# Kernel optimization log

Measured on AMD Instinct MI355X. Metric: run time of the kernel, lower is better.

Reference implementation:

```python
import jax, jax.numpy as jnp
import numpy as np

N = 8192
LATENT_DIM = 64


def setup_inputs() -> dict:
    key = jax.random.key(0)
    kx, ky = jax.random.split(key)
    x = jax.random.normal(kx, (N, LATENT_DIM), dtype=jnp.float32)
    y = jax.random.normal(ky, (N, LATENT_DIM), dtype=jnp.float32)
    return {"x": x, "y": y}


def _rbf_kernel(a, b):
    # Faithful to torch: exp(-mean((a_i - b_j)^2, axis=dim) / dim)
    #                  = exp(-||a_i - b_j||^2 / dim^2)
    # Computed via the expanded-sq-dist identity to avoid the [N, N, dim]
    # tiled intermediate the torch code materializes.
    dim = a.shape[1]
    sq_a = jnp.sum(a * a, axis=1)  # [Na]
    sq_b = jnp.sum(b * b, axis=1)  # [Nb]
    sq_dist = sq_a[:, None] + sq_b[None, :] - 2.0 * (a @ b.T)  # [Na, Nb]
    return jnp.exp(-sq_dist / (dim * dim))


def reference(x, y):
    # MMD with RBF kernel: mean k(x,x) + mean k(y,y) - 2 mean k(x,y)
    kxx = jnp.mean(_rbf_kernel(x, x))
    kyy = jnp.mean(_rbf_kernel(y, y))
    kxy = jnp.mean(_rbf_kernel(x, y))
    return kxx + kyy - 2.0 * kxy
```

## Files before the change

### kernel.cpp

```cpp
#include <hip/hip_runtime.h>
#include <cmath>

#define NPTS 8192
#define DIM 64
#define BT 128

#define LEAF_F   0
#define LEAF_N   (3 * 8192 * 64)
#define ROWS_F   (LEAF_F + LEAF_N)
#define ROWS_N   (3 * 8192)
#define MEANS_F  (ROWS_F + ROWS_N)
#define NX_F     ((MEANS_F + 3 + 3) & ~3)
#define NY_F     (NX_F + 8192)
#define SPLIT_F  (NY_F + 8192)
#define SPLIT_ELEMS (NPTS * DIM)


typedef short bf16x8 __attribute__((ext_vector_type(8)));
typedef float f32x4  __attribute__((ext_vector_type(4)));

__device__ __forceinline__ unsigned short f32_bf16_rne(float f) {
    unsigned u = __float_as_uint(f);
    return (unsigned short)((u + 0x7FFFu + ((u >> 16) & 1u)) >> 16);
}
__device__ __forceinline__ float bf16_f32(unsigned short h) {
    return __uint_as_float(((unsigned)h) << 16);
}

__global__ void prep_kernel(const float* __restrict__ x, const float* __restrict__ y,
                            unsigned short* __restrict__ Xh, unsigned short* __restrict__ Xl,
                            unsigned short* __restrict__ Yh, unsigned short* __restrict__ Yl,
                            float* __restrict__ nx, float* __restrict__ ny) {
    int r = blockIdx.x * 64 + threadIdx.x;
    int isY = r >= NPTS;
    int rr = isY ? r - NPTS : r;
    const float4* Rg = (const float4*)((isY ? y : x) + (size_t)rr * DIM);
    unsigned short* Hh = isY ? Yh : Xh;
    unsigned short* Hl = isY ? Yl : Xl;
    const int t16 = rr >> 4, mrow = rr & 15;
    float s = 0.f;
    #pragma unroll
    for (int k4 = 0; k4 < 16; ++k4) {
        float4 v = Rg[k4];
        ushort4 h, l;
        h.x = f32_bf16_rne(v.x); l.x = f32_bf16_rne(v.x - bf16_f32(h.x));
        h.y = f32_bf16_rne(v.y); l.y = f32_bf16_rne(v.y - bf16_f32(h.y));
        h.z = f32_bf16_rne(v.z); l.z = f32_bf16_rne(v.z - bf16_f32(h.z));
        h.w = f32_bf16_rne(v.w); l.w = f32_bf16_rne(v.w - bf16_f32(h.w));
        int off = t16 * 1024 + (k4 >> 3) * 512 + ((k4 >> 1) & 3) * 128 + mrow * 8 + (k4 & 1) * 4;
        *(ushort4*)(Hh + off) = h;
        *(ushort4*)(Hl + off) = l;
        s = fmaf(v.x, v.x, s); s = fmaf(v.y, v.y, s);
        s = fmaf(v.z, v.z, s); s = fmaf(v.w, v.w, s);
    }
    if (isY) ny[rr] = s; else nx[rr] = s;
}

__global__ __launch_bounds__(512, 4) void mmd_tile_kernel(
    const unsigned short* __restrict__ Xh, const unsigned short* __restrict__ Xl,
    const unsigned short* __restrict__ Yh, const unsigned short* __restrict__ Yl,
    const float* __restrict__ nx, const float* __restrict__ ny,
    float* __restrict__ leafs)
{
    const int gi = blockIdx.x;
    const int gj = blockIdx.y;
    int zz, bx, by;
    if (blockIdx.z == 1) {
        if (gi >= 64) return;
        zz = 2; bx = gi; by = gj;
    } else if (gi > gj) {
        zz = 0; by = gj; bx = gi - 1;
    } else {
        zz = 1; by = gi; bx = gj;
    }

    __shared__ float sqA[BT];
    __shared__ float sqB[BT];
    __shared__ float rowpart[2][BT];
    __shared__ float colpart[4][BT];

    const int t = threadIdx.x;
    const size_t arow = (size_t)by * BT;
    const size_t brow = (size_t)bx * BT;
    const int cb = bx;

    const unsigned short* pAh = (zz == 1) ? Yh : Xh;
    const unsigned short* pAl = (zz == 1) ? Yl : Xl;
    const unsigned short* pBh = (zz == 0) ? Xh : Yh;
    const unsigned short* pBl = (zz == 0) ? Xl : Yl;

    if (t < 256) {
        const float* nA = (zz == 1) ? ny : nx;
        const float* nB = (zz == 0) ? nx : ny;
        if (t < BT) sqA[t] = nA[arow + t];
        else        sqB[t - BT] = nB[brow + t - BT];
    }
    __syncthreads();

    const int lane = t & 63;
    const int wv   = t >> 6;
    const int mrow = lane & 15;
    const int quad = lane >> 4;
    const int rblk = (wv & 3) << 5;
    const int cblk = (wv >> 2) << 6;

    const int aT = by * 8 + (wv & 3) * 2;
    const int bT = bx * 8 + (wv >> 2) * 4;
    const int lsub = quad * 128 + mrow * 8;

    bf16x8 fAh[2][2], fAl[2][2];
    #pragma unroll
    for (int rt = 0; rt < 2; ++rt)
        #pragma unroll
        for (int kc = 0; kc < 2; ++kc) {
            int off = (aT + rt) * 1024 + kc * 512 + lsub;
            fAh[rt][kc] = *(const bf16x8*)(pAh + off);
            fAl[rt][kc] = *(const bf16x8*)(pAl + off);
        }

    f32x4 acc[2][4];
    #pragma unroll
    for (int rt = 0; rt < 2; ++rt)
        #pragma unroll
        for (int ct = 0; ct < 4; ++ct)
            acc[rt][ct] = (f32x4){0.f, 0.f, 0.f, 0.f};

    #pragma unroll
    for (int ct = 0; ct < 4; ++ct) {
        int boff = (bT + ct) * 1024 + lsub;
        bf16x8 bh0 = *(const bf16x8*)(pBh + boff);
        bf16x8 bh1 = *(const bf16x8*)(pBh + boff + 512);
        bf16x8 bl0 = *(const bf16x8*)(pBl + boff);
        bf16x8 bl1 = *(const bf16x8*)(pBl + boff + 512);
        #pragma unroll
        for (int rt = 0; rt < 2; ++rt) {
            f32x4 c = acc[rt][ct];
            c = __builtin_amdgcn_mfma_f32_16x16x32_bf16(fAh[rt][0], bh0, c, 0, 0, 0);
            c = __builtin_amdgcn_mfma_f32_16x16x32_bf16(fAh[rt][0], bl0, c, 0, 0, 0);
            c = __builtin_amdgcn_mfma_f32_16x16x32_bf16(fAl[rt][0], bh0, c, 0, 0, 0);
            c = __builtin_amdgcn_mfma_f32_16x16x32_bf16(fAh[rt][1], bh1, c, 0, 0, 0);
            c = __builtin_amdgcn_mfma_f32_16x16x32_bf16(fAh[rt][1], bl1, c, 0, 0, 0);
            c = __builtin_amdgcn_mfma_f32_16x16x32_bf16(fAl[rt][1], bh1, c, 0, 0, 0);
            acc[rt][ct] = c;
        }
    }

    const float SCL = (float)(-1.4426950408889634 / 4096.0);
    float kk[2][4][4];
    #pragma unroll
    for (int rt = 0; rt < 2; ++rt)
        #pragma unroll
        for (int ct = 0; ct < 4; ++ct)
            #pragma unroll
            for (int i = 0; i < 4; ++i) {
                int row = rblk + rt * 16 + quad * 4 + i;
                int col = cblk + ct * 16 + mrow;
                float d  = acc[rt][ct][i];
                float s2 = sqA[row] + sqB[col];
                float sqd = s2 - 2.0f * d;
                kk[rt][ct][i] = exp2f(sqd * SCL);
            }

    const bool domirror = (zz < 2) && (bx > by);

    float rs[2][4];
    #pragma unroll
    for (int rt = 0; rt < 2; ++rt)
        #pragma unroll
        for (int i = 0; i < 4; ++i)
            rs[rt][i] = (kk[rt][0][i] + kk[rt][1][i]) + (kk[rt][2][i] + kk[rt][3][i]);

    float cs[4];
    if (domirror) {
        #pragma unroll
        for (int ct = 0; ct < 4; ++ct)
            cs[ct] = ((kk[0][ct][0] + kk[0][ct][1]) + (kk[0][ct][2] + kk[0][ct][3]))
                   + ((kk[1][ct][0] + kk[1][ct][1]) + (kk[1][ct][2] + kk[1][ct][3]));
    }

    const int b0 = lane & 1;
    const int b1 = (lane >> 1) & 1;
    const int b2 = (lane >> 2) & 1;
    const int b3 = (lane >> 3) & 1;

    float a4[4];
    #pragma unroll
    for (int i = 0; i < 4; ++i) {
        float snd = b3 ? rs[0][i] : rs[1][i];
        float rcv = __shfl_xor(snd, 8);
        a4[i] = (b3 ? rs[1][i] : rs[0][i]) + rcv;
    }
    float a2[2];
    #pragma unroll
    for (int j = 0; j < 2; ++j) {
        float snd = b2 ? a4[j] : a4[2 + j];
        float rcv = __shfl_xor(snd, 4);
        a2[j] = (b2 ? a4[2 + j] : a4[j]) + rcv;
    }
    {
        float snd = b1 ? a2[0] : a2[1];
        float rcv = __shfl_xor(snd, 2);
        float a1  = (b1 ? a2[1] : a2[0]) + rcv;
        float r64 = a1 + __shfl_xor(a1, 1);
        if (b0 == 0)
            rowpart[wv >> 2][rblk + b3 * 16 + quad * 4 + b2 * 2 + b1] = r64;
    }

    if (domirror) {
        const int b4 = (lane >> 4) & 1;
        const int b5 = (lane >> 5) & 1;
        float c2[2];
        #pragma unroll
        for (int j = 0; j < 2; ++j) {
            float snd = b4 ? cs[j] : cs[2 + j];
            float rcv = __shfl_xor(snd, 16);
            c2[j] = (b4 ? cs[2 + j] : cs[j]) + rcv;
        }
        float snd = b5 ? c2[0] : c2[1];
        float rcv = __shfl_xor(snd, 32);
        float c1  = (b5 ? c2[1] : c2[0]) + rcv;
        colpart[wv & 3][cblk + (b4 * 2 + b5) * 16 + mrow] = c1;
    }
    __syncthreads();

    if (t < BT) {
        leafs[((size_t)zz * 64 + cb) * 8192 + arow + t] = rowpart[0][t] + rowpart[1][t];
        if (domirror) {
            leafs[((size_t)zz * 64 + by) * 8192 + brow + t] =
                (colpart[0][t] + colpart[1][t]) + (colpart[2][t] + colpart[3][t]);
        }
    }
}

__global__ void rowsum_kernel(const float* __restrict__ leafs, float* __restrict__ rowsums) {
    const int t = threadIdx.x;
    const int tid = blockIdx.x * 256 + t;
    const int z = tid >> 13;
    const int r = tid & 8191;
    const float* base = leafs + ((size_t)z * 64) * 8192 + r;
    float v[64];
    #pragma unroll
    for (int cbi = 0; cbi < 64; ++cbi) v[cbi] = base[(size_t)cbi * 8192];
    #pragma unroll
    for (int n = 32; n >= 1; n >>= 1)
        #pragma unroll
        for (int i = 0; i < 64; ++i)
            if (i < n) v[i] = v[2*i] + v[2*i+1];
    rowsums[tid] = v[0];
}

__global__ void colsum_kernel(const float* __restrict__ rowsums, float* __restrict__ means) {
    __shared__ float L[256];
    const int z = blockIdx.x;
    const int t = threadIdx.x;
    const float4* src = (const float4*)(rowsums + z * 8192);
    float w[32];
    #pragma unroll
    for (int i = 0; i < 8; ++i) {
        float4 q = src[t * 8 + i];
        w[4*i+0] = q.x; w[4*i+1] = q.y; w[4*i+2] = q.z; w[4*i+3] = q.w;
    }
    #pragma unroll
    for (int n = 16; n >= 1; n >>= 1)
        #pragma unroll
        for (int i = 0; i < 32; ++i)
            if (i < n) w[i] = w[2*i] + w[2*i+1];
    L[t] = w[0];
    __syncthreads();
    for (int n = 128; n >= 1; n >>= 1) {
        float u = 0.f;
        if (t < n) u = L[2*t] + L[2*t+1];
        __syncthreads();
        if (t < n) L[t] = u;
        __syncthreads();
    }
    if (t == 0) means[z] = L[0] * (1.0f / 67108864.0f);
}

__global__ void combine_kernel(const float* __restrict__ means, float* __restrict__ out) {
    float t1 = means[0] + means[1];
    out[0] = t1 - 2.0f * means[2];
}

extern "C" void kernel_launch(void* const* d_in, const int* in_sizes, int n_in,
                              void* d_out, int out_size, void* d_ws, size_t ws_size,
                              hipStream_t stream) {
    const float* x = (const float*)d_in[0];
    const float* y = (const float*)d_in[1];
    float* wsf     = (float*)d_ws;
    float* leafs   = wsf + LEAF_F;
    float* rowsums = wsf + ROWS_F;
    float* means   = wsf + MEANS_F;
    float* nx      = wsf + NX_F;
    float* ny      = wsf + NY_F;
    unsigned short* Xh = (unsigned short*)(wsf + SPLIT_F);
    unsigned short* Xl = Xh + SPLIT_ELEMS;
    unsigned short* Yh = Xl + SPLIT_ELEMS;
    unsigned short* Yl = Yh + SPLIT_ELEMS;

    prep_kernel<<<256, 64, 0, stream>>>(x, y, Xh, Xl, Yh, Yl, nx, ny);
    dim3 grid(65, 64, 2);
    mmd_tile_kernel<<<grid, 512, 0, stream>>>(Xh, Xl, Yh, Yl, nx, ny, leafs);
    rowsum_kernel<<<96, 256, 0, stream>>>(leafs, rowsums);
    colsum_kernel<<<3, 256, 0, stream>>>(rowsums, means);
    combine_kernel<<<1, 1, 0, stream>>>(means, (float*)d_out);
}
```

Before: 146.5 us.

## Interleave MFMA with exp epilogue, hardware exp2, swizzle shuffles, fuse final reductions

The tile kernel now computes exp and row/column partial sums per column tile right after its MFMAs, so the full accumulator array no longer has to stay live. Squared norms are loaded directly into registers instead of through shared memory, which removes a barrier. exp2f is replaced with the raw v_exp_f32 instruction, and most xor shuffles are replaced with ds_swizzle. The colsum and combine kernels are merged into a single one-block launch, removing one kernel launch at the cost of serializing the three reductions.

```diff
diff --git a/kernel.cpp b/kernel.cpp
--- a/kernel.cpp
+++ b/kernel.cpp
@@ -26,6 +26,22 @@
 __device__ __forceinline__ float bf16_f32(unsigned short h) {
     return __uint_as_float(((unsigned)h) << 16);
 }
+
+__device__ __forceinline__ float exp2_hw(float x) {
+#if __has_builtin(__builtin_amdgcn_exp2f)
+    return __builtin_amdgcn_exp2f(x);
+#else
+    float r;
+    asm("v_exp_f32 %0, %1" : "=v"(r) : "v"(x));
+    return r;
+#endif
+}
+
+#define SWZ_XOR1(x)  __int_as_float(__builtin_amdgcn_ds_swizzle(__float_as_int(x), 0x041F))
+#define SWZ_XOR2(x)  __int_as_float(__builtin_amdgcn_ds_swizzle(__float_as_int(x), 0x081F))
+#define SWZ_XOR4(x)  __int_as_float(__builtin_amdgcn_ds_swizzle(__float_as_int(x), 0x101F))
+#define SWZ_XOR8(x)  __int_as_float(__builtin_amdgcn_ds_swizzle(__float_as_int(x), 0x201F))
+#define SWZ_XOR16(x) __int_as_float(__builtin_amdgcn_ds_swizzle(__float_as_int(x), 0x401F))
 
 __global__ void prep_kernel(const float* __restrict__ x, const float* __restrict__ y,
                             unsigned short* __restrict__ Xh, unsigned short* __restrict__ Xl,
@@ -74,8 +90,6 @@
         zz = 1; by = gi; bx = gj;
     }
 
-    __shared__ float sqA[BT];
-    __shared__ float sqB[BT];
     __shared__ float rowpart[2][BT];
     __shared__ float colpart[4][BT];
 
@@ -88,14 +102,8 @@
     const unsigned short* pAl = (zz == 1) ? Yl : Xl;
     const unsigned short* pBh = (zz == 0) ? Xh : Yh;
     const unsigned short* pBl = (zz == 0) ? Xl : Yl;
-
-    if (t < 256) {
-        const float* nA = (zz == 1) ? ny : nx;
-        const float* nB = (zz == 0) ? nx : ny;
-        if (t < BT) sqA[t] = nA[arow + t];
-        else        sqB[t - BT] = nB[brow + t - BT];
-    }
-    __syncthreads();
+    const float* nA = (zz == 1) ? ny : nx;
+    const float* nB = (zz == 0) ? nx : ny;
 
     const int lane = t & 63;
     const int wv   = t >> 6;
@@ -108,6 +116,19 @@
     const int bT = bx * 8 + (wv >> 2) * 4;
     const int lsub = quad * 128 + mrow * 8;
 
+    const bool domirror = (zz < 2) && (bx > by);
+
+    float sa[8];
+    #pragma unroll
+    for (int rt = 0; rt < 2; ++rt)
+        #pragma unroll
+        for (int i = 0; i < 4; ++i)
+            sa[rt * 4 + i] = nA[arow + rblk + rt * 16 + quad * 4 + i];
+    float sb[4];
+    #pragma unroll
+    for (int ct = 0; ct < 4; ++ct)
+        sb[ct] = nB[brow + cblk + ct * 16 + mrow];
+
     bf16x8 fAh[2][2], fAl[2][2];
     #pragma unroll
     for (int rt = 0; rt < 2; ++rt)
@@ -118,12 +139,10 @@
             fAl[rt][kc] = *(const bf16x8*)(pAl + off);
         }
 
-    f32x4 acc[2][4];
-    #pragma unroll
-    for (int rt = 0; rt < 2; ++rt)
-        #pragma unroll
-        for (int ct = 0; ct < 4; ++ct)
-            acc[rt][ct] = (f32x4){0.f, 0.f, 0.f, 0.f};
+    const float SCL = (float)(-1.4426950408889634 / 4096.0);
+    float rs01[2][4] = {{0.f,0.f,0.f,0.f},{0.f,0.f,0.f,0.f}};
+    float rs23[2][4] = {{0.f,0.f,0.f,0.f},{0.f,0.f,0.f,0.f}};
+    float cs[4];
 
     #pragma unroll
     for (int ct = 0; ct < 4; ++ct) {
@@ -132,51 +151,50 @@
         bf16x8 bh1 = *(const bf16x8*)(pBh + boff + 512);
         bf16x8 bl0 = *(const bf16x8*)(pBl + boff);
         bf16x8 bl1 = *(const bf16x8*)(pBl + boff + 512);
-        #pragma unroll
-        for (int rt = 0; rt < 2; ++rt) {
-            f32x4 c = acc[rt][ct];
-            c = __builtin_amdgcn_mfma_f32_16x16x32_bf16(fAh[rt][0], bh0, c, 0, 0, 0);
-            c = __builtin_amdgcn_mfma_f32_16x16x32_bf16(fAh[rt][0], bl0, c, 0, 0, 0);
-            c = __builtin_amdgcn_mfma_f32_16x16x32_bf16(fAl[rt][0], bh0, c, 0, 0, 0);
-            c = __builtin_amdgcn_mfma_f32_16x16x32_bf16(fAh[rt][1], bh1, c, 0, 0, 0);
-            c = __builtin_amdgcn_mfma_f32_16x16x32_bf16(fAh[rt][1], bl1, c, 0, 0, 0);
-            c = __builtin_amdgcn_mfma_f32_16x16x32_bf16(fAl[rt][1], bh1, c, 0, 0, 0);
-            acc[rt][ct] = c;
-        }
-    }
-
-    const float SCL = (float)(-1.4426950408889634 / 4096.0);
-    float kk[2][4][4];
+
+        f32x4 c0 = (f32x4){0.f, 0.f, 0.f, 0.f};
+        f32x4 c1 = (f32x4){0.f, 0.f, 0.f, 0.f};
+        c0 = __builtin_amdgcn_mfma_f32_16x16x32_bf16(fAh[0][0], bh0, c0, 0, 0, 0);
+        c0 = __builtin_amdgcn_mfma_f32_16x16x32_bf16(fAh[0][0], bl0, c0, 0, 0, 0);
+        c0 = __builtin_amdgcn_mfma_f32_16x16x32_bf16(fAl[0][0], bh0, c0, 0, 0, 0);
+        c0 = __builtin_amdgcn_mfma_f32_16x16x32_bf16(fAh[0][1], bh1, c0, 0, 0, 0);
+        c0 = __builtin_amdgcn_mfma_f32_16x16x32_bf16(fAh[0][1], bl1, c0, 0, 0, 0);
+        c0 = __builtin_amdgcn_mfma_f32_16x16x32_bf16(fAl[0][1], bh1, c0, 0, 0, 0);
+        c1 = __builtin_amdgcn_mfma_f32_16x16x32_bf16(fAh[1][0], bh0, c1, 0, 0, 0);
+        c1 = __builtin_amdgcn_mfma_f32_16x16x32_bf16(fAh[1][0], bl0, c1, 0, 0, 0);
+        c1 = __builtin_amdgcn_mfma_f32_16x16x32_bf16(fAl[1][0], bh0, c1, 0, 0, 0);
+        c1 = __builtin_amdgcn_mfma_f32_16x16x32_bf16(fAh[1][1], bh1, c1, 0, 0, 0);
+        c1 = __builtin_amdgcn_mfma_f32_16x16x32_bf16(fAh[1][1], bl1, c1, 0, 0, 0);
+        c1 = __builtin_amdgcn_mfma_f32_16x16x32_bf16(fAl[1][1], bh1, c1, 0, 0, 0);
+
+        float k0[4], k1[4];
+        #pragma unroll
+        for (int i = 0; i < 4; ++i) {
+            float d0  = c0[i];
+            float s20 = sa[i] + sb[ct];
+            k0[i] = exp2_hw((s20 - 2.0f * d0) * SCL);
+            float d1  = c1[i];
+            float s21 = sa[4 + i] + sb[ct];
+            k1[i] = exp2_hw((s21 - 2.0f * d1) * SCL);
+        }
+        if (ct < 2) {
+            #pragma unroll
+            for (int i = 0; i < 4; ++i) { rs01[0][i] += k0[i]; rs01[1][i] += k1[i]; }
+        } else {
+            #pragma unroll
+            for (int i = 0; i < 4; ++i) { rs23[0][i] += k0[i]; rs23[1][i] += k1[i]; }
+        }
+        if (domirror)
+            cs[ct] = ((k0[0] + k0[1]) + (k0[2] + k0[3]))
+                   + ((k1[0] + k1[1]) + (k1[2] + k1[3]));
+    }
+
+    float rs[2][4];
     #pragma unroll
     for (int rt = 0; rt < 2; ++rt)
         #pragma unroll
-        for (int ct = 0; ct < 4; ++ct)
-            #pragma unroll
-            for (int i = 0; i < 4; ++i) {
-                int row = rblk + rt * 16 + quad * 4 + i;
-                int col = cblk + ct * 16 + mrow;
-                float d  = acc[rt][ct][i];
-                float s2 = sqA[row] + sqB[col];
-                float sqd = s2 - 2.0f * d;
-                kk[rt][ct][i] = exp2f(sqd * SCL);
-            }
-
-    const bool domirror = (zz < 2) && (bx > by);
-
-    float rs[2][4];
-    #pragma unroll
-    for (int rt = 0; rt < 2; ++rt)
-        #pragma unroll
         for (int i = 0; i < 4; ++i)
-            rs[rt][i] = (kk[rt][0][i] + kk[rt][1][i]) + (kk[rt][2][i] + kk[rt][3][i]);
-
-    float cs[4];
-    if (domirror) {
-        #pragma unroll
-        for (int ct = 0; ct < 4; ++ct)
-            cs[ct] = ((kk[0][ct][0] + kk[0][ct][1]) + (kk[0][ct][2] + kk[0][ct][3]))
-                   + ((kk[1][ct][0] + kk[1][ct][1]) + (kk[1][ct][2] + kk[1][ct][3]));
-    }
+            rs[rt][i] = rs01[rt][i] + rs23[rt][i];
 
     const int b0 = lane & 1;
     const int b1 = (lane >> 1) & 1;
@@ -187,21 +205,21 @@
     #pragma unroll
     for (int i = 0; i < 4; ++i) {
         float snd = b3 ? rs[0][i] : rs[1][i];
-        float rcv = __shfl_xor(snd, 8);
+        float rcv = SWZ_XOR8(snd);
         a4[i] = (b3 ? rs[1][i] : rs[0][i]) + rcv;
     }
     float a2[2];
     #pragma unroll
     for (int j = 0; j < 2; ++j) {
         float snd = b2 ? a4[j] : a4[2 + j];
-        float rcv = __shfl_xor(snd, 4);
+        float rcv = SWZ_XOR4(snd);
         a2[j] = (b2 ? a4[2 + j] : a4[j]) + rcv;
     }
     {
         float snd = b1 ? a2[0] : a2[1];
-        float rcv = __shfl_xor(snd, 2);
+        float rcv = SWZ_XOR2(snd);
         float a1  = (b1 ? a2[1] : a2[0]) + rcv;
-        float r64 = a1 + __shfl_xor(a1, 1);
+        float r64 = a1 + SWZ_XOR1(a1);
         if (b0 == 0)
             rowpart[wv >> 2][rblk + b3 * 16 + quad * 4 + b2 * 2 + b1] = r64;
     }
@@ -213,13 +231,13 @@
         #pragma unroll
         for (int j = 0; j < 2; ++j) {
             float snd = b4 ? cs[j] : cs[2 + j];
-            float rcv = __shfl_xor(snd, 16);
+            float rcv = SWZ_XOR16(snd);
             c2[j] = (b4 ? cs[2 + j] : cs[j]) + rcv;
         }
         float snd = b5 ? c2[0] : c2[1];
         float rcv = __shfl_xor(snd, 32);
-        float c1  = (b5 ? c2[1] : c2[0]) + rcv;
-        colpart[wv & 3][cblk + (b4 * 2 + b5) * 16 + mrow] = c1;
+        float c1v = (b5 ? c2[1] : c2[0]) + rcv;
+        colpart[wv & 3][cblk + (b4 * 2 + b5) * 16 + mrow] = c1v;
     }
     __syncthreads();
 
@@ -249,37 +267,39 @@
     rowsums[tid] = v[0];
 }
 
-__global__ void colsum_kernel(const float* __restrict__ rowsums, float* __restrict__ means) {
+__global__ void colsum_kernel(const float* __restrict__ rowsums, float* __restrict__ out) {
     __shared__ float L[256];
-    const int z = blockIdx.x;
+    __shared__ float m[3];
     const int t = threadIdx.x;
-    const float4* src = (const float4*)(rowsums + z * 8192);
-    float w[32];
-    #pragma unroll
-    for (int i = 0; i < 8; ++i) {
-        float4 q = src[t * 8 + i];
-        w[4*i+0] = q.x; w[4*i+1] = q.y; w[4*i+2] = q.z; w[4*i+3] = q.w;
-    }
-    #pragma unroll
-    for (int n = 16; n >= 1; n >>= 1)
-        #pragma unroll
-        for (int i = 0; i < 32; ++i)
-            if (i < n) w[i] = w[2*i] + w[2*i+1];
-    L[t] = w[0];
-    __syncthreads();
-    for (int n = 128; n >= 1; n >>= 1) {
-        float u = 0.f;
-        if (t < n) u = L[2*t] + L[2*t+1];
+    for (int z = 0; z < 3; ++z) {
+        const float4* src = (const float4*)(rowsums + z * 8192);
+        float w[32];
+        #pragma unroll
+        for (int i = 0; i < 8; ++i) {
+            float4 q = src[t * 8 + i];
+            w[4*i+0] = q.x; w[4*i+1] = q.y; w[4*i+2] = q.z; w[4*i+3] = q.w;
+        }
+        #pragma unroll
+        for (int n = 16; n >= 1; n >>= 1)
+            #pragma unroll
+            for (int i = 0; i < 32; ++i)
+                if (i < n) w[i] = w[2*i] + w[2*i+1];
+        L[t] = w[0];
         __syncthreads();
-        if (t < n) L[t] = u;
+        for (int n = 128; n >= 1; n >>= 1) {
+            float u = 0.f;
+            if (t < n) u = L[2*t] + L[2*t+1];
+            __syncthreads();
+            if (t < n) L[t] = u;
+            __syncthreads();
+        }
+        if (t == 0) m[z] = L[0] * (1.0f / 67108864.0f);
         __syncthreads();
     }
-    if (t == 0) means[z] = L[0] * (1.0f / 67108864.0f);
-}
-
-__global__ void combine_kernel(const float* __restrict__ means, float* __restrict__ out) {
-    float t1 = means[0] + means[1];
-    out[0] = t1 - 2.0f * means[2];
+    if (t == 0) {
+        float t1 = m[0] + m[1];
+        out[0] = t1 - 2.0f * m[2];
+    }
 }
 
 extern "C" void kernel_launch(void* const* d_in, const int* in_sizes, int n_in,
@@ -290,7 +310,6 @@
     float* wsf     = (float*)d_ws;
     float* leafs   = wsf + LEAF_F;
     float* rowsums = wsf + ROWS_F;
-    float* means   = wsf + MEANS_F;
     float* nx      = wsf + NX_F;
     float* ny      = wsf + NY_F;
     unsigned short* Xh = (unsigned short*)(wsf + SPLIT_F);
@@ -302,6 +321,5 @@
     dim3 grid(65, 64, 2);
     mmd_tile_kernel<<<grid, 512, 0, stream>>>(Xh, Xl, Yh, Yl, nx, ny, leafs);
     rowsum_kernel<<<96, 256, 0, stream>>>(leafs, rowsums);
-    colsum_kernel<<<3, 256, 0, stream>>>(rowsums, means);
-    combine_kernel<<<1, 1, 0, stream>>>(means, (float*)d_out);
-}
+    colsum_kernel<<<1, 256, 0, stream>>>(rowsums, (float*)d_out);
+}
```

Result: faster. 140.6 us (-4.0%).
